# Optimization experiments

Hardware: AMD Instinct MI355X
Metric: run time of the kernel (lower is better)

Reference implementation:

```python
import jax, jax.numpy as jnp
import numpy as np

N, E, D_IN, HID, HEADS = 50000, 800000, 128, 32, 8
NEG_SLOPE = 0.2


def gat_conv(x, src, dst, W_src, W_dst, a_src, a_dst, b, heads, ch, concat):
    n = x.shape[0]
    hs = (x @ W_src).reshape(n, heads, ch)  # source-side features [N,H,C]
    hd = (x @ W_dst).reshape(n, heads, ch)  # dest-side features   [N,H,C]
    alpha_s = jnp.einsum('nhc,hc->nh', hs, a_src)  # [N,H]
    alpha_d = jnp.einsum('nhc,hc->nh', hd, a_dst)  # [N,H]
    e = jax.nn.leaky_relu(alpha_s[src] + alpha_d[dst], NEG_SLOPE)  # [E,H]
    # segment softmax over edges grouped by destination node
    m = jax.ops.segment_max(e, dst, num_segments=n)
    m = jnp.where(jnp.isfinite(m), m, 0.0)
    e = jnp.exp(e - jax.lax.stop_gradient(m)[dst])
    denom = jax.ops.segment_sum(e, dst, num_segments=n)
    alpha = e / (denom[dst] + 1e-16)  # [E,H]
    # weighted scatter-aggregate of source features to destinations
    out = jax.ops.segment_sum(hs[src] * alpha[:, :, None], dst, num_segments=n)  # [N,H,C]
    out = out.reshape(n, heads * ch) if concat else out.mean(axis=1)
    return out + b


def setup_inputs() -> dict:
    key = jax.random.key(0)
    ks = jax.random.split(key, 12)
    glorot = lambda k, shape: jax.random.normal(k, shape, jnp.float32) * np.sqrt(2.0 / (shape[0] + shape[-1]))
    x = jax.random.normal(ks[0], (N, D_IN), jnp.float32)
    edge_index = jax.random.randint(ks[1], (2, E), 0, N, jnp.int64)
    return {
        'x': x,
        'edge_index': edge_index,
        'W1_src': glorot(ks[2], (D_IN, HEADS * HID)),
        'W1_dst': glorot(ks[3], (D_IN, HEADS * HID)),
        'a1_src': glorot(ks[4], (HEADS, HID)),
        'a1_dst': glorot(ks[5], (HEADS, HID)),
        'b1': jnp.zeros((HEADS * HID,), jnp.float32),
        'W2_src': glorot(ks[6], (HEADS * HID, HID)),
        'W2_dst': glorot(ks[7], (HEADS * HID, HID)),
        'a2_src': glorot(ks[8], (1, HID)),
        'a2_dst': glorot(ks[9], (1, HID)),
        'b2': jnp.zeros((HID,), jnp.float32),
    }


def reference(x, edge_index, W1_src, W1_dst, a1_src, a1_dst, b1,
              W2_src, W2_dst, a2_src, a2_dst, b2):
    src, dst = edge_index[0], edge_index[1]
    h = gat_conv(x, src, dst, W1_src, W1_dst, a1_src, a1_dst, b1, HEADS, HID, True)
    h = jax.nn.relu(h)
    out = gat_conv(h, src, dst, W2_src, W2_dst, a2_src, a2_dst, b2, 1, HID, True)
    return out
```

## Files before the change

### kernel.cpp

```cpp
#include <hip/hip_runtime.h>
#include <hip/hip_bf16.h>

#define NEG_SLOPE 0.2f

typedef unsigned int uint;
typedef unsigned short ushort;
typedef __attribute__((ext_vector_type(8))) short short8;
typedef __attribute__((ext_vector_type(4))) float floatx4;

static __device__ __forceinline__ ushort f2bf(float f) {
    uint u = __float_as_uint(f);
    uint r = (u + 0x7fffu + ((u >> 16) & 1u)) >> 16;
    return (ushort)r;
}
static __device__ __forceinline__ float bf2f(uint s) {
    return __uint_as_float(s << 16);
}

__global__ __launch_bounds__(256) void hist_kernel(
    const int* __restrict__ dst, int* __restrict__ deg, int E) {
    int e = blockIdx.x * blockDim.x + threadIdx.x;
    if (e < E) atomicAdd(&deg[dst[e]], 1);
}

__global__ __launch_bounds__(256) void scan_block(
    const int* __restrict__ deg, int* __restrict__ rs,
    int* __restrict__ bsum, int n) {
    __shared__ int sh[256];
    int tid = threadIdx.x;
    int i = blockIdx.x * 256 + tid;
    sh[tid] = (i < n) ? deg[i] : 0;
    __syncthreads();
    for (int off = 1; off < 256; off <<= 1) {
        int t = (tid >= off) ? sh[tid - off] : 0;
        __syncthreads();
        sh[tid] += t;
        __syncthreads();
    }
    if (i < n) rs[i] = sh[tid];
    if (tid == 255) bsum[blockIdx.x] = sh[255];
}

__global__ __launch_bounds__(256) void rs_kernel(
    const int* __restrict__ deg, const int* __restrict__ bsum,
    int* __restrict__ rs, int* __restrict__ cursor, int n, int E, int nb) {
    __shared__ int sh[256];
    int tid = threadIdx.x;
    int own = (tid < nb) ? bsum[tid] : 0;
    sh[tid] = own;
    __syncthreads();
    for (int off = 1; off < 256; off <<= 1) {
        int t = (tid >= off) ? sh[tid - off] : 0;
        __syncthreads();
        sh[tid] += t;
        __syncthreads();
    }
    int boff = sh[blockIdx.x] - ((blockIdx.x < nb) ? bsum[blockIdx.x] : 0);
    __syncthreads();
    int i = blockIdx.x * 256 + tid;
    if (i < n) {
        int v = rs[i] - deg[i] + boff;
        rs[i] = v;
        cursor[i] = v;
    }
    if (i == 0) rs[n] = E;
}

__global__ __launch_bounds__(256) void fill_kernel(
    const int* __restrict__ src, const int* __restrict__ dst,
    int* __restrict__ cursor, int* __restrict__ csr_src, int E) {
    int e = blockIdx.x * blockDim.x + threadIdx.x;
    if (e >= E) return;
    int d = dst[e];
    int pos = atomicAdd(&cursor[d], 1);
    csr_src[pos] = src[e];
}

__global__ __launch_bounds__(256) void prep_weights(
    const float* __restrict__ W1_src, const float* __restrict__ W2_src,
    const float* __restrict__ W1_dst, const float* __restrict__ a1_dst,
    const float* __restrict__ W2_dst, const float* __restrict__ a2_dst,
    ushort* __restrict__ W1t, ushort* __restrict__ W2t,
    float* __restrict__ wc1, float* __restrict__ wc2) {
    int i = blockIdx.x * blockDim.x + threadIdx.x;
    if (i < 32768) {
        int nc = i & 255, k = i >> 8;
        W1t[nc * 128 + k] = f2bf(W1_src[k * 256 + nc]);
    } else if (i < 32768 + 8192) {
        int i2 = i - 32768;
        int c = i2 & 31, k = i2 >> 5;
        W2t[c * 256 + k] = f2bf(W2_src[k * 32 + c]);
    } else if (i < 32768 + 8192 + 1024) {
        int i3 = i - 32768 - 8192;
        int k = i3 >> 3, h = i3 & 7;
        float s = 0.f;
#pragma unroll
        for (int c = 0; c < 32; ++c)
            s += W1_dst[k * 256 + h * 32 + c] * a1_dst[h * 32 + c];
        wc1[i3] = s;
    } else if (i < 32768 + 8192 + 1024 + 256) {
        int k = i - 32768 - 8192 - 1024;
        float s = 0.f;
#pragma unroll
        for (int c = 0; c < 32; ++c)
            s += W2_dst[k * 32 + c] * a2_dst[c];
        wc2[k] = s;
    }
}

__global__ __launch_bounds__(256) void gemm1_mfma(
    const float* __restrict__ x, const ushort* __restrict__ W1t,
    const float* __restrict__ a_src, const float* __restrict__ wc1,
    ushort* __restrict__ hs1b, float* __restrict__ as1,
    float* __restrict__ ad1, int n) {
    __shared__ ushort At[128 * 128];
    __shared__ ushort Out[128 * 128];
    int mblk = blockIdx.x >> 1, nhalf = blockIdx.x & 1;
    int m0 = mblk * 128;
    int tid = threadIdx.x;
#pragma unroll
    for (int i = 0; i < 8; ++i) {
        int id = tid + i * 256;
        int m = id >> 4, c = id & 15;
        int gm = m0 + m;
        uint4 pk = {0, 0, 0, 0};
        if (gm < n) {
            const float4* xp = (const float4*)(x + (size_t)gm * 128 + c * 8);
            float4 v0 = xp[0], v1 = xp[1];
            pk.x = (uint)f2bf(v0.x) | ((uint)f2bf(v0.y) << 16);
            pk.y = (uint)f2bf(v0.z) | ((uint)f2bf(v0.w) << 16);
            pk.z = (uint)f2bf(v1.x) | ((uint)f2bf(v1.y) << 16);
            pk.w = (uint)f2bf(v1.z) | ((uint)f2bf(v1.w) << 16);
        }
        *(uint4*)(At + m * 128 + ((c ^ (m & 15)) * 8)) = pk;
    }
    __syncthreads();
    int wid = tid >> 6, lane = tid & 63;
    int q = lane >> 4, l16 = lane & 15;
    int wm = (wid >> 1) * 64;
    int wn = (wid & 1) * 64;
    int gn0 = nhalf * 128 + wn;
    floatx4 z = {0.f, 0.f, 0.f, 0.f};
    floatx4 acc[4][4];
#pragma unroll
    for (int mt = 0; mt < 4; ++mt)
#pragma unroll
        for (int nt = 0; nt < 4; ++nt) acc[mt][nt] = z;
#pragma unroll
    for (int s = 0; s < 4; ++s) {
        short8 af[4], bf[4];
#pragma unroll
        for (int mt = 0; mt < 4; ++mt) {
            int row = wm + mt * 16 + l16;
            int c = s * 4 + q;
            af[mt] = *(const short8*)(At + row * 128 + ((c ^ (row & 15)) * 8));
        }
#pragma unroll
        for (int nt = 0; nt < 4; ++nt) {
            int col = gn0 + nt * 16 + l16;
            bf[nt] = *(const short8*)(W1t + col * 128 + s * 32 + q * 8);
        }
#pragma unroll
        for (int mt = 0; mt < 4; ++mt)
#pragma unroll
            for (int nt = 0; nt < 4; ++nt)
                acc[mt][nt] = __builtin_amdgcn_mfma_f32_16x16x32_bf16(
                    af[mt], bf[nt], acc[mt][nt], 0, 0, 0);
    }
#pragma unroll
    for (int mt = 0; mt < 4; ++mt)
#pragma unroll
        for (int nt = 0; nt < 4; ++nt) {
            floatx4 a = acc[mt][nt];
            int colL = wn + nt * 16 + l16;
#pragma unroll
            for (int r = 0; r < 4; ++r) {
                int rowL = wm + mt * 16 + q * 4 + r;
                Out[rowL * 128 + colL] = f2bf(a[r]);
            }
        }
    __syncthreads();
#pragma unroll
    for (int i = 0; i < 8; ++i) {
        int id = tid + i * 256;
        int m = id >> 4, c8 = id & 15;
        int gm = m0 + m;
        if (gm < n) {
            uint4 v = *(uint4*)(Out + m * 128 + c8 * 8);
            *(uint4*)(hs1b + (size_t)gm * 256 + nhalf * 128 + c8 * 8) = v;
        }
    }
#pragma unroll
    for (int i = 0; i < 2; ++i) {
        int id = tid + i * 256;
        int m = id & 127, hl = id >> 7;
        int gm = m0 + m;
        if (gm < n) {
            int h = nhalf * 4 + hl;
            const ushort* row = Out + m * 128 + hl * 32;
            const float* av = a_src + h * 32;
            float s = 0.f;
#pragma unroll
            for (int c = 0; c < 32; ++c) s += bf2f(row[c]) * av[c];
            as1[(size_t)gm * 8 + h] = s;
        }
    }
    if (nhalf == 0) {
#pragma unroll
        for (int i = 0; i < 4; ++i) {
            int id = tid + i * 256;
            int m = id & 127, h = id >> 7;
            int gm = m0 + m;
            if (gm < n) {
                float s = 0.f;
                for (int c = 0; c < 16; ++c) {
                    const ushort* p = At + m * 128 + ((c ^ (m & 15)) * 8);
#pragma unroll
                    for (int jj = 0; jj < 8; ++jj)
                        s += bf2f(p[jj]) * wc1[(c * 8 + jj) * 8 + h];
                }
                ad1[(size_t)gm * 8 + h] = s;
            }
        }
    }
}

__global__ __launch_bounds__(256) void gather1(
    const int* __restrict__ csr_src, const int* __restrict__ rs,
    const ushort* __restrict__ hs1b, const float* __restrict__ as1,
    const float* __restrict__ ad1, const float* __restrict__ b1,
    ushort* __restrict__ h1b, int n) {
    int gid = blockIdx.x * blockDim.x + threadIdx.x;
    int node = gid >> 6;
    int lane = threadIdx.x & 63;
    if (node >= n) return;
    int j = lane >> 5, l = lane & 31;
    int h = l >> 2;
    float ad_v = ad1[node * 8 + h];
    int start = rs[node], cnt = rs[node + 1] - start;
    float acc0 = 0.f, acc1 = 0.f, acc2 = 0.f, acc3 = 0.f;
    float acc4 = 0.f, acc5 = 0.f, acc6 = 0.f, acc7 = 0.f;
    float dacc = 0.f;
    int i = j;
    for (; i + 2 < cnt; i += 4) {
        int sA = csr_src[start + i];
        int sB = csr_src[start + i + 2];
        float tA = as1[sA * 8 + h] + ad_v;
        float tB = as1[sB * 8 + h] + ad_v;
        uint4 vA = *(const uint4*)(hs1b + (size_t)sA * 256 + l * 8);
        uint4 vB = *(const uint4*)(hs1b + (size_t)sB * 256 + l * 8);
        tA = (tA >= 0.f) ? tA : NEG_SLOPE * tA;
        tB = (tB >= 0.f) ? tB : NEG_SLOPE * tB;
        float wA = __expf(tA);
        float wB = __expf(tB);
        acc0 += bf2f(vA.x & 0xffffu) * wA + bf2f(vB.x & 0xffffu) * wB;
        acc1 += bf2f(vA.x >> 16) * wA + bf2f(vB.x >> 16) * wB;
        acc2 += bf2f(vA.y & 0xffffu) * wA + bf2f(vB.y & 0xffffu) * wB;
        acc3 += bf2f(vA.y >> 16) * wA + bf2f(vB.y >> 16) * wB;
        acc4 += bf2f(vA.z & 0xffffu) * wA + bf2f(vB.z & 0xffffu) * wB;
        acc5 += bf2f(vA.z >> 16) * wA + bf2f(vB.z >> 16) * wB;
        acc6 += bf2f(vA.w & 0xffffu) * wA + bf2f(vB.w & 0xffffu) * wB;
        acc7 += bf2f(vA.w >> 16) * wA + bf2f(vB.w >> 16) * wB;
        dacc += wA + wB;
    }
    for (; i < cnt; i += 2) {
        int s = csr_src[start + i];
        float t = as1[s * 8 + h] + ad_v;
        uint4 v = *(const uint4*)(hs1b + (size_t)s * 256 + l * 8);
        t = (t >= 0.f) ? t : NEG_SLOPE * t;
        float w = __expf(t);
        acc0 += bf2f(v.x & 0xffffu) * w;
        acc1 += bf2f(v.x >> 16) * w;
        acc2 += bf2f(v.y & 0xffffu) * w;
        acc3 += bf2f(v.y >> 16) * w;
        acc4 += bf2f(v.z & 0xffffu) * w;
        acc5 += bf2f(v.z >> 16) * w;
        acc6 += bf2f(v.w & 0xffffu) * w;
        acc7 += bf2f(v.w >> 16) * w;
        dacc += w;
    }
    acc0 += __shfl_xor(acc0, 32, 64);
    acc1 += __shfl_xor(acc1, 32, 64);
    acc2 += __shfl_xor(acc2, 32, 64);
    acc3 += __shfl_xor(acc3, 32, 64);
    acc4 += __shfl_xor(acc4, 32, 64);
    acc5 += __shfl_xor(acc5, 32, 64);
    acc6 += __shfl_xor(acc6, 32, 64);
    acc7 += __shfl_xor(acc7, 32, 64);
    dacc += __shfl_xor(dacc, 32, 64);
    if (j == 0) {
        float inv = 1.f / (dacc + 1e-16f);
        float4 b0 = ((const float4*)b1)[l * 2];
        float4 b4 = ((const float4*)b1)[l * 2 + 1];
        float o0 = fmaxf(fmaf(acc0, inv, b0.x), 0.f);
        float o1 = fmaxf(fmaf(acc1, inv, b0.y), 0.f);
        float o2 = fmaxf(fmaf(acc2, inv, b0.z), 0.f);
        float o3 = fmaxf(fmaf(acc3, inv, b0.w), 0.f);
        float o4 = fmaxf(fmaf(acc4, inv, b4.x), 0.f);
        float o5 = fmaxf(fmaf(acc5, inv, b4.y), 0.f);
        float o6 = fmaxf(fmaf(acc6, inv, b4.z), 0.f);
        float o7 = fmaxf(fmaf(acc7, inv, b4.w), 0.f);
        uint4 pk;
        pk.x = (uint)f2bf(o0) | ((uint)f2bf(o1) << 16);
        pk.y = (uint)f2bf(o2) | ((uint)f2bf(o3) << 16);
        pk.z = (uint)f2bf(o4) | ((uint)f2bf(o5) << 16);
        pk.w = (uint)f2bf(o6) | ((uint)f2bf(o7) << 16);
        *(uint4*)(h1b + (size_t)node * 256 + l * 8) = pk;
    }
}

__global__ __launch_bounds__(256) void gemm2_mfma(
    const ushort* __restrict__ h1b, const ushort* __restrict__ W2t,
    const float* __restrict__ a2_src, const float* __restrict__ wc2,
    ushort* __restrict__ hs2b, float* __restrict__ as2,
    float* __restrict__ ad2, int n) {
    __shared__ ushort At[128 * 256];
    __shared__ ushort Out[128 * 32];
    int m0 = blockIdx.x * 128;
    int tid = threadIdx.x;
#pragma unroll
    for (int i = 0; i < 16; ++i) {
        int id = tid + i * 256;
        int m = id >> 5, c = id & 31;
        int gm = m0 + m;
        uint4 v = {0, 0, 0, 0};
        if (gm < n) v = *(const uint4*)(h1b + (size_t)gm * 256 + c * 8);
        *(uint4*)(At + m * 256 + ((c ^ (m & 15)) * 8)) = v;
    }
    __syncthreads();
    int wid = tid >> 6, lane = tid & 63;
    int q = lane >> 4, l16 = lane & 15;
    int wm = wid * 32;
    floatx4 z = {0.f, 0.f, 0.f, 0.f};
    floatx4 acc[2][2] = {{z, z}, {z, z}};
#pragma unroll
    for (int s = 0; s < 8; ++s) {
        short8 af[2], bf[2];
#pragma unroll
        for (int mt = 0; mt < 2; ++mt) {
            int row = wm + mt * 16 + l16;
            int c = s * 4 + q;
            af[mt] = *(const short8*)(At + row * 256 + ((c ^ (row & 15)) * 8));
        }
#pragma unroll
        for (int nt = 0; nt < 2; ++nt) {
            int col = nt * 16 + l16;
            bf[nt] = *(const short8*)(W2t + col * 256 + s * 32 + q * 8);
        }
#pragma unroll
        for (int mt = 0; mt < 2; ++mt)
#pragma unroll
            for (int nt = 0; nt < 2; ++nt)
                acc[mt][nt] = __builtin_amdgcn_mfma_f32_16x16x32_bf16(
                    af[mt], bf[nt], acc[mt][nt], 0, 0, 0);
    }
#pragma unroll
    for (int mt = 0; mt < 2; ++mt)
#pragma unroll
        for (int nt = 0; nt < 2; ++nt) {
            floatx4 a = acc[mt][nt];
            int colL = nt * 16 + l16;
#pragma unroll
            for (int r = 0; r < 4; ++r) {
                int rowL = wm + mt * 16 + q * 4 + r;
                Out[rowL * 32 + colL] = f2bf(a[r]);
            }
        }
    __syncthreads();
#pragma unroll
    for (int i = 0; i < 2; ++i) {
        int id = tid + i * 256;
        int c4 = id & 3, m = id >> 2;
        int gm = m0 + m;
        if (gm < n)
            *(uint4*)(hs2b + (size_t)gm * 32 + c4 * 8) =
                *(uint4*)(Out + m * 32 + c4 * 8);
    }
    if (tid < 128) {
        int gm = m0 + tid;
        if (gm < n) {
            float s = 0.f;
#pragma unroll
            for (int c2 = 0; c2 < 32; ++c2)
                s += bf2f(Out[tid * 32 + c2]) * a2_src[c2];
            as2[gm] = s;
        }
    } else {
        int m = tid - 128, gm = m0 + m;
        if (gm < n) {
            float s = 0.f;
            for (int c = 0; c < 32; ++c) {
                const ushort* p = At + m * 256 + ((c ^ (m & 15)) * 8);
#pragma unroll
                for (int jj = 0; jj < 8; ++jj)
                    s += bf2f(p[jj]) * wc2[c * 8 + jj];
            }
            ad2[gm] = s;
        }
    }
}

__global__ __launch_bounds__(256) void gather2(
    const int* __restrict__ csr_src, const int* __restrict__ rs,
    const ushort* __restrict__ hs2b, const float* __restrict__ as2,
    const float* __restrict__ ad2, const float* __restrict__ b2,
    float* __restrict__ out, int n) {
    int gid = blockIdx.x * blockDim.x + threadIdx.x;
    int node = gid >> 6;
    int lane = threadIdx.x & 63;
    if (node >= n) return;
    int g = lane >> 3, l = lane & 7;
    float ad_v = ad2[node];
    int start = rs[node], cnt = rs[node + 1] - start;
    float a0 = 0.f, a1 = 0.f, a2 = 0.f, a3 = 0.f, dacc = 0.f;
    for (int i = g; i < cnt; i += 8) {
        int s = csr_src[start + i];
        float t = as2[s] + ad_v;
        t = (t >= 0.f) ? t : NEG_SLOPE * t;
        float w = __expf(t);
        uint2 v = *(const uint2*)(hs2b + (size_t)s * 32 + l * 4);
        a0 += bf2f(v.x & 0xffffu) * w;
        a1 += bf2f(v.x >> 16) * w;
        a2 += bf2f(v.y & 0xffffu) * w;
        a3 += bf2f(v.y >> 16) * w;
        dacc += w;
    }
#pragma unroll
    for (int m = 8; m <= 32; m <<= 1) {
        a0 += __shfl_xor(a0, m, 64);
        a1 += __shfl_xor(a1, m, 64);
        a2 += __shfl_xor(a2, m, 64);
        a3 += __shfl_xor(a3, m, 64);
        dacc += __shfl_xor(dacc, m, 64);
    }
    if (g == 0) {
        float inv = 1.f / (dacc + 1e-16f);
        float4 bv = ((const float4*)b2)[l];
        float4 o;
        o.x = fmaf(a0, inv, bv.x);
        o.y = fmaf(a1, inv, bv.y);
        o.z = fmaf(a2, inv, bv.z);
        o.w = fmaf(a3, inv, bv.w);
        *(float4*)(out + (size_t)node * 32 + l * 4) = o;
    }
}

extern "C" void kernel_launch(void* const* d_in, const int* in_sizes, int n_in,
                              void* d_out, int out_size, void* d_ws, size_t ws_size,
                              hipStream_t stream) {
    const float* x      = (const float*)d_in[0];
    const int*   eidx   = (const int*)d_in[1];
    const float* W1_src = (const float*)d_in[2];
    const float* W1_dst = (const float*)d_in[3];
    const float* a1_src = (const float*)d_in[4];
    const float* a1_dst = (const float*)d_in[5];
    const float* b1     = (const float*)d_in[6];
    const float* W2_src = (const float*)d_in[7];
    const float* W2_dst = (const float*)d_in[8];
    const float* a2_src = (const float*)d_in[9];
    const float* a2_dst = (const float*)d_in[10];
    const float* b2     = (const float*)d_in[11];

    const int n = in_sizes[0] / 128;
    const int E = in_sizes[1] / 2;
    const int* srcp = eidx;
    const int* dstp = eidx + E;
    const int nb = (n + 255) / 256;

    char* ws = (char*)d_ws;
    size_t o = 0;
    auto alloc = [&](size_t bytes) {
        void* p = ws + o;
        o += (bytes + 255) & ~(size_t)255;
        return p;
    };
    ushort* W1t  = (ushort*)alloc(256 * 128 * 2);
    ushort* W2t  = (ushort*)alloc(32 * 256 * 2);
    ushort* hs1b = (ushort*)alloc((size_t)n * 256 * 2);
    ushort* h1b  = (ushort*)alloc((size_t)n * 256 * 2);
    ushort* hs2b = (ushort*)alloc((size_t)n * 32 * 2);
    float* as1 = (float*)alloc((size_t)n * 8 * 4);
    float* ad1 = (float*)alloc((size_t)n * 8 * 4);
    float* as2 = (float*)alloc((size_t)n * 4);
    float* ad2 = (float*)alloc((size_t)n * 4);
    float* wc1 = (float*)alloc(1024 * 4);
    float* wc2 = (float*)alloc(256 * 4);
    int* deg     = (int*)alloc((size_t)n * 4);
    int* rs      = (int*)alloc(((size_t)n + 1) * 4);
    int* cursor  = (int*)alloc((size_t)n * 4);
    int* bsum    = (int*)alloc(256 * 4);
    int* csr_src = (int*)alloc((size_t)E * 4);

    hipMemsetAsync(deg, 0, (size_t)n * sizeof(int), stream);

    hist_kernel<<<(E + 255) / 256, 256, 0, stream>>>(dstp, deg, E);
    scan_block<<<nb, 256, 0, stream>>>(deg, rs, bsum, n);
    rs_kernel<<<nb, 256, 0, stream>>>(deg, bsum, rs, cursor, n, E, nb);
    fill_kernel<<<(E + 255) / 256, 256, 0, stream>>>(srcp, dstp, cursor,
                                                     csr_src, E);

    prep_weights<<<(32768 + 8192 + 1024 + 256 + 255) / 256, 256, 0, stream>>>(
        W1_src, W2_src, W1_dst, a1_dst, W2_dst, a2_dst, W1t, W2t, wc1, wc2);

    gemm1_mfma<<<((n + 127) / 128) * 2, 256, 0, stream>>>(
        x, W1t, a1_src, wc1, hs1b, as1, ad1, n);
    gather1<<<(n + 3) / 4, 256, 0, stream>>>(
        csr_src, rs, hs1b, as1, ad1, b1, h1b, n);

    gemm2_mfma<<<(n + 127) / 128, 256, 0, stream>>>(
        h1b, W2t, a2_src, wc2, hs2b, as2, ad2, n);
    gather2<<<(n + 3) / 4, 256, 0, stream>>>(
        csr_src, rs, hs2b, as2, ad2, b2, (float*)d_out, n);
}
```

Before: 326.4 us.

## Fuse CSR build kernels and merge gemm1 column halves per block

Merges the degree histogram with weight preparation into one launch, and replaces the two-kernel scan with a single kernel that chains block offsets through flags. Vectorises edge reads (two edges per thread) in the histogram and fill kernels. gemm1 now computes both 128-column halves in one block, so x is loaded and converted once and ad1 needs no conditional branch. Fewer launches cut launch overhead, at the cost of half as many gemm1 blocks and a spin-wait scan that assumes all earlier blocks are resident.

```diff
diff --git a/kernel.cpp b/kernel.cpp
--- a/kernel.cpp
+++ b/kernel.cpp
@@ -17,72 +17,26 @@
     return __uint_as_float(s << 16);
 }
 
-__global__ __launch_bounds__(256) void hist_kernel(
-    const int* __restrict__ dst, int* __restrict__ deg, int E) {
-    int e = blockIdx.x * blockDim.x + threadIdx.x;
-    if (e < E) atomicAdd(&deg[dst[e]], 1);
-}
-
-__global__ __launch_bounds__(256) void scan_block(
-    const int* __restrict__ deg, int* __restrict__ rs,
-    int* __restrict__ bsum, int n) {
-    __shared__ int sh[256];
-    int tid = threadIdx.x;
-    int i = blockIdx.x * 256 + tid;
-    sh[tid] = (i < n) ? deg[i] : 0;
-    __syncthreads();
-    for (int off = 1; off < 256; off <<= 1) {
-        int t = (tid >= off) ? sh[tid - off] : 0;
-        __syncthreads();
-        sh[tid] += t;
-        __syncthreads();
-    }
-    if (i < n) rs[i] = sh[tid];
-    if (tid == 255) bsum[blockIdx.x] = sh[255];
-}
-
-__global__ __launch_bounds__(256) void rs_kernel(
-    const int* __restrict__ deg, const int* __restrict__ bsum,
-    int* __restrict__ rs, int* __restrict__ cursor, int n, int E, int nb) {
-    __shared__ int sh[256];
-    int tid = threadIdx.x;
-    int own = (tid < nb) ? bsum[tid] : 0;
-    sh[tid] = own;
-    __syncthreads();
-    for (int off = 1; off < 256; off <<= 1) {
-        int t = (tid >= off) ? sh[tid - off] : 0;
-        __syncthreads();
-        sh[tid] += t;
-        __syncthreads();
-    }
-    int boff = sh[blockIdx.x] - ((blockIdx.x < nb) ? bsum[blockIdx.x] : 0);
-    __syncthreads();
-    int i = blockIdx.x * 256 + tid;
-    if (i < n) {
-        int v = rs[i] - deg[i] + boff;
-        rs[i] = v;
-        cursor[i] = v;
-    }
-    if (i == 0) rs[n] = E;
-}
-
-__global__ __launch_bounds__(256) void fill_kernel(
-    const int* __restrict__ src, const int* __restrict__ dst,
-    int* __restrict__ cursor, int* __restrict__ csr_src, int E) {
-    int e = blockIdx.x * blockDim.x + threadIdx.x;
-    if (e >= E) return;
-    int d = dst[e];
-    int pos = atomicAdd(&cursor[d], 1);
-    csr_src[pos] = src[e];
-}
-
-__global__ __launch_bounds__(256) void prep_weights(
+__global__ __launch_bounds__(256) void histprep_kernel(
+    const int* __restrict__ dst, int* __restrict__ deg, int E, int HB,
     const float* __restrict__ W1_src, const float* __restrict__ W2_src,
     const float* __restrict__ W1_dst, const float* __restrict__ a1_dst,
     const float* __restrict__ W2_dst, const float* __restrict__ a2_dst,
     ushort* __restrict__ W1t, ushort* __restrict__ W2t,
     float* __restrict__ wc1, float* __restrict__ wc2) {
-    int i = blockIdx.x * blockDim.x + threadIdx.x;
+    if (blockIdx.x < (uint)HB) {
+        int i = blockIdx.x * blockDim.x + threadIdx.x;
+        int e0 = i * 2;
+        if (e0 + 1 < E) {
+            int2 d2 = ((const int2*)dst)[i];
+            atomicAdd(&deg[d2.x], 1);
+            atomicAdd(&deg[d2.y], 1);
+        } else if (e0 < E) {
+            atomicAdd(&deg[dst[e0]], 1);
+        }
+        return;
+    }
+    int i = (blockIdx.x - HB) * blockDim.x + threadIdx.x;
     if (i < 32768) {
         int nc = i & 255, k = i >> 8;
         W1t[nc * 128 + k] = f2bf(W1_src[k * 256 + nc]);
@@ -108,6 +62,70 @@
     }
 }
 
+__global__ __launch_bounds__(256) void scanrs_kernel(
+    const int* __restrict__ deg, int* __restrict__ rs,
+    int* __restrict__ cursor, int* __restrict__ agg,
+    int* __restrict__ flag, int n, int E) {
+    __shared__ int sh[256];
+    int tid = threadIdx.x;
+    int c = blockIdx.x;
+    int i = c * 256 + tid;
+    int d = (i < n) ? deg[i] : 0;
+    sh[tid] = d;
+    __syncthreads();
+    for (int off = 1; off < 256; off <<= 1) {
+        int t = (tid >= off) ? sh[tid - off] : 0;
+        __syncthreads();
+        sh[tid] += t;
+        __syncthreads();
+    }
+    int incl = sh[tid];
+    if (tid == 255) {
+        agg[c] = incl;
+        __threadfence();
+        __hip_atomic_store(&flag[c], 1, __ATOMIC_RELEASE,
+                           __HIP_MEMORY_SCOPE_AGENT);
+    }
+    int vt = 0;
+    if (tid < c) {
+        while (__hip_atomic_load(&flag[tid], __ATOMIC_ACQUIRE,
+                                 __HIP_MEMORY_SCOPE_AGENT) == 0) {}
+        vt = agg[tid];
+    }
+    __syncthreads();
+    sh[tid] = vt;
+    __syncthreads();
+    for (int off = 128; off > 0; off >>= 1) {
+        if (tid < off) sh[tid] += sh[tid + off];
+        __syncthreads();
+    }
+    int boff = sh[0];
+    if (i < n) {
+        int v = incl - d + boff;
+        rs[i] = v;
+        cursor[i] = v;
+    }
+    if (c == 0 && tid == 0) rs[n] = E;
+}
+
+__global__ __launch_bounds__(256) void fill_kernel(
+    const int* __restrict__ src, const int* __restrict__ dst,
+    int* __restrict__ cursor, int* __restrict__ csr_src, int E) {
+    int i = blockIdx.x * blockDim.x + threadIdx.x;
+    int e0 = i * 2;
+    if (e0 + 1 < E) {
+        int2 d2 = ((const int2*)dst)[i];
+        int2 s2 = ((const int2*)src)[i];
+        int p0 = atomicAdd(&cursor[d2.x], 1);
+        int p1 = atomicAdd(&cursor[d2.y], 1);
+        csr_src[p0] = s2.x;
+        csr_src[p1] = s2.y;
+    } else if (e0 < E) {
+        int pos = atomicAdd(&cursor[dst[e0]], 1);
+        csr_src[pos] = src[e0];
+    }
+}
+
 __global__ __launch_bounds__(256) void gemm1_mfma(
     const float* __restrict__ x, const ushort* __restrict__ W1t,
     const float* __restrict__ a_src, const float* __restrict__ wc1,
@@ -115,8 +133,7 @@
     float* __restrict__ ad1, int n) {
     __shared__ ushort At[128 * 128];
     __shared__ ushort Out[128 * 128];
-    int mblk = blockIdx.x >> 1, nhalf = blockIdx.x & 1;
-    int m0 = mblk * 128;
+    int m0 = blockIdx.x * 128;
     int tid = threadIdx.x;
 #pragma unroll
     for (int i = 0; i < 8; ++i) {
@@ -139,88 +156,89 @@
     int q = lane >> 4, l16 = lane & 15;
     int wm = (wid >> 1) * 64;
     int wn = (wid & 1) * 64;
-    int gn0 = nhalf * 128 + wn;
     floatx4 z = {0.f, 0.f, 0.f, 0.f};
-    floatx4 acc[4][4];
-#pragma unroll
-    for (int mt = 0; mt < 4; ++mt)
-#pragma unroll
-        for (int nt = 0; nt < 4; ++nt) acc[mt][nt] = z;
-#pragma unroll
-    for (int s = 0; s < 4; ++s) {
-        short8 af[4], bf[4];
-#pragma unroll
-        for (int mt = 0; mt < 4; ++mt) {
-            int row = wm + mt * 16 + l16;
-            int c = s * 4 + q;
-            af[mt] = *(const short8*)(At + row * 128 + ((c ^ (row & 15)) * 8));
-        }
-#pragma unroll
-        for (int nt = 0; nt < 4; ++nt) {
-            int col = gn0 + nt * 16 + l16;
-            bf[nt] = *(const short8*)(W1t + col * 128 + s * 32 + q * 8);
-        }
+    for (int nhalf = 0; nhalf < 2; ++nhalf) {
+        int gn0 = nhalf * 128 + wn;
+        floatx4 acc[4][4];
 #pragma unroll
         for (int mt = 0; mt < 4; ++mt)
 #pragma unroll
-            for (int nt = 0; nt < 4; ++nt)
-                acc[mt][nt] = __builtin_amdgcn_mfma_f32_16x16x32_bf16(
-                    af[mt], bf[nt], acc[mt][nt], 0, 0, 0);
-    }
-#pragma unroll
-    for (int mt = 0; mt < 4; ++mt)
-#pragma unroll
-        for (int nt = 0; nt < 4; ++nt) {
-            floatx4 a = acc[mt][nt];
-            int colL = wn + nt * 16 + l16;
-#pragma unroll
-            for (int r = 0; r < 4; ++r) {
-                int rowL = wm + mt * 16 + q * 4 + r;
-                Out[rowL * 128 + colL] = f2bf(a[r]);
-            }
-        }
-    __syncthreads();
-#pragma unroll
-    for (int i = 0; i < 8; ++i) {
+            for (int nt = 0; nt < 4; ++nt) acc[mt][nt] = z;
+#pragma unroll
+        for (int s = 0; s < 4; ++s) {
+            short8 af[4], bf[4];
+#pragma unroll
+            for (int mt = 0; mt < 4; ++mt) {
+                int row = wm + mt * 16 + l16;
+                int c = s * 4 + q;
+                af[mt] = *(const short8*)(At + row * 128 + ((c ^ (row & 15)) * 8));
+            }
+#pragma unroll
+            for (int nt = 0; nt < 4; ++nt) {
+                int col = gn0 + nt * 16 + l16;
+                bf[nt] = *(const short8*)(W1t + col * 128 + s * 32 + q * 8);
+            }
+#pragma unroll
+            for (int mt = 0; mt < 4; ++mt)
+#pragma unroll
+                for (int nt = 0; nt < 4; ++nt)
+                    acc[mt][nt] = __builtin_amdgcn_mfma_f32_16x16x32_bf16(
+                        af[mt], bf[nt], acc[mt][nt], 0, 0, 0);
+        }
+        __syncthreads();
+#pragma unroll
+        for (int mt = 0; mt < 4; ++mt)
+#pragma unroll
+            for (int nt = 0; nt < 4; ++nt) {
+                floatx4 a = acc[mt][nt];
+                int colL = wn + nt * 16 + l16;
+#pragma unroll
+                for (int r = 0; r < 4; ++r) {
+                    int rowL = wm + mt * 16 + q * 4 + r;
+                    Out[rowL * 128 + colL] = f2bf(a[r]);
+                }
+            }
+        __syncthreads();
+#pragma unroll
+        for (int i = 0; i < 8; ++i) {
+            int id = tid + i * 256;
+            int m = id >> 4, c8 = id & 15;
+            int gm = m0 + m;
+            if (gm < n) {
+                uint4 v = *(uint4*)(Out + m * 128 + c8 * 8);
+                *(uint4*)(hs1b + (size_t)gm * 256 + nhalf * 128 + c8 * 8) = v;
+            }
+        }
+#pragma unroll
+        for (int i = 0; i < 2; ++i) {
+            int id = tid + i * 256;
+            int m = id & 127, hl = id >> 7;
+            int gm = m0 + m;
+            if (gm < n) {
+                int h = nhalf * 4 + hl;
+                const ushort* row = Out + m * 128 + hl * 32;
+                const float* av = a_src + h * 32;
+                float s = 0.f;
+#pragma unroll
+                for (int c = 0; c < 32; ++c) s += bf2f(row[c]) * av[c];
+                as1[(size_t)gm * 8 + h] = s;
+            }
+        }
+    }
+#pragma unroll
+    for (int i = 0; i < 4; ++i) {
         int id = tid + i * 256;
-        int m = id >> 4, c8 = id & 15;
+        int m = id & 127, h = id >> 7;
         int gm = m0 + m;
         if (gm < n) {
-            uint4 v = *(uint4*)(Out + m * 128 + c8 * 8);
-            *(uint4*)(hs1b + (size_t)gm * 256 + nhalf * 128 + c8 * 8) = v;
-        }
-    }
-#pragma unroll
-    for (int i = 0; i < 2; ++i) {
-        int id = tid + i * 256;
-        int m = id & 127, hl = id >> 7;
-        int gm = m0 + m;
-        if (gm < n) {
-            int h = nhalf * 4 + hl;
-            const ushort* row = Out + m * 128 + hl * 32;
-            const float* av = a_src + h * 32;
             float s = 0.f;
-#pragma unroll
-            for (int c = 0; c < 32; ++c) s += bf2f(row[c]) * av[c];
-            as1[(size_t)gm * 8 + h] = s;
-        }
-    }
-    if (nhalf == 0) {
-#pragma unroll
-        for (int i = 0; i < 4; ++i) {
-            int id = tid + i * 256;
-            int m = id & 127, h = id >> 7;
-            int gm = m0 + m;
-            if (gm < n) {
-                float s = 0.f;
-                for (int c = 0; c < 16; ++c) {
-                    const ushort* p = At + m * 128 + ((c ^ (m & 15)) * 8);
-#pragma unroll
-                    for (int jj = 0; jj < 8; ++jj)
-                        s += bf2f(p[jj]) * wc1[(c * 8 + jj) * 8 + h];
-                }
-                ad1[(size_t)gm * 8 + h] = s;
-            }
+            for (int c = 0; c < 16; ++c) {
+                const ushort* p = At + m * 128 + ((c ^ (m & 15)) * 8);
+#pragma unroll
+                for (int jj = 0; jj < 8; ++jj)
+                    s += bf2f(p[jj]) * wc1[(c * 8 + jj) * 8 + h];
+            }
+            ad1[(size_t)gm * 8 + h] = s;
         }
     }
 }
@@ -485,24 +503,26 @@
     float* ad2 = (float*)alloc((size_t)n * 4);
     float* wc1 = (float*)alloc(1024 * 4);
     float* wc2 = (float*)alloc(256 * 4);
-    int* deg     = (int*)alloc((size_t)n * 4);
+    int* csrmeta = (int*)alloc(((size_t)n + 512) * 4);
+    int* deg  = csrmeta;
+    int* agg  = csrmeta + n;
+    int* flag = csrmeta + n + 256;
     int* rs      = (int*)alloc(((size_t)n + 1) * 4);
     int* cursor  = (int*)alloc((size_t)n * 4);
-    int* bsum    = (int*)alloc(256 * 4);
     int* csr_src = (int*)alloc((size_t)E * 4);
 
-    hipMemsetAsync(deg, 0, (size_t)n * sizeof(int), stream);
-
-    hist_kernel<<<(E + 255) / 256, 256, 0, stream>>>(dstp, deg, E);
-    scan_block<<<nb, 256, 0, stream>>>(deg, rs, bsum, n);
-    rs_kernel<<<nb, 256, 0, stream>>>(deg, bsum, rs, cursor, n, E, nb);
-    fill_kernel<<<(E + 255) / 256, 256, 0, stream>>>(srcp, dstp, cursor,
-                                                     csr_src, E);
-
-    prep_weights<<<(32768 + 8192 + 1024 + 256 + 255) / 256, 256, 0, stream>>>(
-        W1_src, W2_src, W1_dst, a1_dst, W2_dst, a2_dst, W1t, W2t, wc1, wc2);
-
-    gemm1_mfma<<<((n + 127) / 128) * 2, 256, 0, stream>>>(
+    hipMemsetAsync(csrmeta, 0, ((size_t)n + 512) * sizeof(int), stream);
+
+    const int HB = (E / 2 + 255) / 256;
+    const int PB = (32768 + 8192 + 1024 + 256 + 255) / 256;
+    histprep_kernel<<<HB + PB, 256, 0, stream>>>(
+        dstp, deg, E, HB, W1_src, W2_src, W1_dst, a1_dst, W2_dst, a2_dst,
+        W1t, W2t, wc1, wc2);
+    scanrs_kernel<<<nb, 256, 0, stream>>>(deg, rs, cursor, agg, flag, n, E);
+    fill_kernel<<<(E / 2 + 255) / 256, 256, 0, stream>>>(srcp, dstp, cursor,
+                                                         csr_src, E);
+
+    gemm1_mfma<<<(n + 127) / 128, 256, 0, stream>>>(
         x, W1t, a1_src, wc1, hs1b, as1, ad1, n);
     gather1<<<(n + 3) / 4, 256, 0, stream>>>(
         csr_src, rs, hs1b, as1, ad1, b1, h1b, n);
```

After: 323.4 us. No clear change (-0.9%).
